# Kernel optimization log

Hardware: AMD Instinct MI355X
Metric: run time of the kernel (lower is better)

The kernel has to match this reference:

```python
import jax, jax.numpy as jnp
import numpy as np

N, B, F_DIM, K, DEG = 102400, 64, 64, 16, 8
E = N * DEG
PER_G = N // B  # equal-size graphs -> to_dense_batch is a reshape
EPS = 1e-15


def setup_inputs() -> dict:
    key = jax.random.key(0)
    k1, k2, k3, k4 = jax.random.split(key, 4)
    node_attr = jax.random.normal(k1, (N, F_DIM), dtype=jnp.float32)
    W = jax.random.normal(k2, (F_DIM, K), dtype=jnp.float32) * 0.1
    b = jnp.zeros((K,), dtype=jnp.float32)
    row = jax.random.randint(k3, (E,), 0, N)
    # receivers constrained to the sender's graph (block structure)
    col = (row // PER_G) * PER_G + jax.random.randint(k4, (E,), 0, PER_G)
    edge_index = jnp.stack([row, col]).astype(jnp.int32)
    batch = jnp.repeat(jnp.arange(B, dtype=jnp.int32), PER_G)
    return {"node_attr": node_attr, "W": W, "b": b,
            "edge_index": edge_index, "batch": batch, "num_graphs": B}


def reference(node_attr, W, b, edge_index, batch, num_graphs):
    n, f = node_attr.shape
    k = W.shape[1]
    per_g = n // num_graphs
    # selection = softmax(Linear(node_attr))            [N, K]
    sel = jax.nn.softmax(node_attr @ W + b, axis=-1)
    s = sel.reshape(num_graphs, per_g, k)               # to_dense_batch (equal graphs)
    row, col = edge_index[0], edge_index[1]
    # edge_pooling: outer product per edge, scatter-add by graph of sender
    assign_edge = sel[row][:, :, None] * sel[col][:, None, :]       # [E, K, K]
    dense_adj = jax.ops.segment_sum(assign_edge, batch[row], num_segments=num_graphs)  # [B, K, K]
    # normalize_adj (remove_self_loops=False)
    d = jnp.sqrt(dense_adj.sum(-1))[:, None, :] + EPS   # [B, 1, K]
    dense_adj = dense_adj / d / jnp.swapaxes(d, 1, 2)
    # mincut loss
    mincut_num = jnp.trace(dense_adj, axis1=1, axis2=2)             # [B]
    deg = jax.ops.segment_sum(jnp.ones((row.shape[0],), node_attr.dtype), row, num_segments=n)
    d_flat = deg.reshape(num_graphs, per_g)                          # [B, Nmax]
    # trace(S^T diag(d) S) = sum_n d_n * sum_k s_nk^2
    mincut_den = jnp.einsum('bn,bnk,bnk->b', d_flat, s, s)
    mincut_loss = jnp.mean(-(mincut_num / mincut_den))
    # orthogonality loss
    ss = jnp.einsum('bnk,bnl->bkl', s, s)                            # [B, K, K]
    ss_norm = jnp.linalg.norm(ss, axis=(-2, -1), keepdims=True)
    i_s = jnp.eye(k, dtype=ss.dtype)
    ortho = jnp.linalg.norm(ss / ss_norm - i_s / jnp.sqrt(jnp.asarray(k, ss.dtype)), axis=(-2, -1))
    ortho_loss = jnp.mean(ortho)
    # node_pooling: scatter of sel ⊗ node_attr by graph, flattened over (B, K)
    x = node_attr.reshape(num_graphs, per_g, f)
    cluster_node_attr = jnp.einsum('bnk,bnf->bkf', s, x).reshape(num_graphs * k, f)
    return cluster_node_attr, dense_adj, mincut_loss, ortho_loss
```

## Files before the change

### kernel.cpp

```cpp
#include <hip/hip_runtime.h>

#define F_DIMC 64
#define K_DIMC 16
#define NGRAPH 64
#define NXCD 8
#define SX_SPLIT 16
#define NB_SEL 400
#define NB_CHUNK 256
#define NB_ZERO 64
#define CHUNK_I4 800
#define ADJ_BLOCKS 256
#define ADJ_OFF (NGRAPH * K_DIMC * F_DIMC)
#define LOSS_OFF (ADJ_OFF + NGRAPH * K_DIMC * K_DIMC)
#define ZERO_BYTES 394240

typedef __attribute__((ext_vector_type(8))) short s16x8;
typedef __attribute__((ext_vector_type(4))) float f32x4;


__device__ inline unsigned short f2bf(float f) {
    unsigned u = __builtin_bit_cast(unsigned, f);
    u += 0x7fffu + ((u >> 16) & 1u);
    return (unsigned short)(u >> 16);
}

__global__ __launch_bounds__(256) void k_sel_hist(const float* __restrict__ node_attr,
                                                  const float* __restrict__ W,
                                                  const float* __restrict__ bias,
                                                  const int* __restrict__ row,
                                                  float* __restrict__ sel,
                                                  int* __restrict__ blockhist,
                                                  float4* __restrict__ zdst,
                                                  int N, int perG) {
    int t = threadIdx.x;
    if (blockIdx.x < NB_SEL) {
        __shared__ float sW[K_DIMC][F_DIMC];
        __shared__ float sb[K_DIMC];
        for (int idx = t; idx < F_DIMC * K_DIMC; idx += 256) {
            int f = idx / K_DIMC, k = idx % K_DIMC;
            sW[k][f] = W[idx];
        }
        if (t < K_DIMC) sb[t] = bias[t];
        __syncthreads();
        int n = blockIdx.x * 256 + t;
        if (n >= N) return;

        const float4* xr = (const float4*)(node_attr + (size_t)n * F_DIMC);
        float4 x[F_DIMC / 4];
#pragma unroll
        for (int f4 = 0; f4 < F_DIMC / 4; ++f4) x[f4] = xr[f4];

        float logits[K_DIMC];
#pragma unroll
        for (int k = 0; k < K_DIMC; ++k) {
            const float4* wk = (const float4*)&sW[k][0];
            float acc = sb[k];
#pragma unroll
            for (int f4 = 0; f4 < F_DIMC / 4; ++f4) {
                float4 w = wk[f4];
                acc += x[f4].x * w.x + x[f4].y * w.y + x[f4].z * w.z + x[f4].w * w.w;
            }
            logits[k] = acc;
        }
        float m = logits[0];
#pragma unroll
        for (int k = 1; k < K_DIMC; ++k) m = fmaxf(m, logits[k]);
        float sum = 0.f;
#pragma unroll
        for (int k = 0; k < K_DIMC; ++k) {
            float e = __expf(logits[k] - m);
            logits[k] = e;
            sum += e;
        }
        float inv = 1.f / sum;
        float4* sd = (float4*)(sel + (size_t)n * K_DIMC);
#pragma unroll
        for (int k4 = 0; k4 < K_DIMC / 4; ++k4) {
            float4 v;
            v.x = logits[4 * k4 + 0] * inv;
            v.y = logits[4 * k4 + 1] * inv;
            v.z = logits[4 * k4 + 2] * inv;
            v.w = logits[4 * k4 + 3] * inv;
            sd[k4] = v;
        }
    } else if (blockIdx.x < NB_SEL + NB_CHUNK) {
        __shared__ int lh[NGRAPH];
        int h = blockIdx.x - NB_SEL;
        if (t < NGRAPH) lh[t] = 0;
        __syncthreads();
        for (int i = t; i < CHUNK_I4; i += 256) {
            int4 r4 = ((const int4*)row)[h * CHUNK_I4 + i];
            atomicAdd(&lh[r4.x / perG], 1);
            atomicAdd(&lh[r4.y / perG], 1);
            atomicAdd(&lh[r4.z / perG], 1);
            atomicAdd(&lh[r4.w / perG], 1);
        }
        __syncthreads();
        if (t < NGRAPH) blockhist[h * NGRAPH + t] = lh[t];
    } else {
        int z = blockIdx.x - NB_SEL - NB_CHUNK;
        for (int i = z * 256 + t; i < ZERO_BYTES / 16; i += NB_ZERO * 256)
            zdst[i] = make_float4(0.f, 0.f, 0.f, 0.f);
    }
}

__global__ __launch_bounds__(256) void k_chunkscan(const int* __restrict__ blockhist,
                                                   int* __restrict__ chunkbase,
                                                   int* __restrict__ gtot) {
    int g = blockIdx.x;
    int t = threadIdx.x;
    int lane = t & 63;
    int wid = t >> 6;
    int v = blockhist[t * NGRAPH + g];
    int s = v;
#pragma unroll
    for (int d = 1; d < 64; d <<= 1) {
        int o = __shfl_up(s, d);
        if (lane >= d) s += o;
    }
    __shared__ int wsum[4];
    if (lane == 63) wsum[wid] = s;
    __syncthreads();
    int pre = 0;
#pragma unroll
    for (int w = 0; w < 4; ++w) pre += (w < wid) ? wsum[w] : 0;
    int incl = s + pre;
    chunkbase[t * NGRAPH + g] = incl - v;
    if (t == 255) gtot[g] = incl;
}

__global__ __launch_bounds__(256) void k_scatter_sx(const int* __restrict__ row,
                                                    const int* __restrict__ col,
                                                    const int* __restrict__ gtot,
                                                    const int* __restrict__ chunkbase,
                                                    int* __restrict__ offsets,
                                                    uint2* __restrict__ sorted,
                                                    const float* __restrict__ sel,
                                                    const float* __restrict__ x,
                                                    float* __restrict__ ssbuf,
                                                    float* __restrict__ sxbuf,
                                                    int perG) {
    int b = blockIdx.x;
    int r5 = b % 5;
    int t = threadIdx.x;
    if (r5 == 0) {
        __shared__ int base_[NGRAPH];
        __shared__ int lcnt[NGRAPH];
        int h = b / 5;
        if (t < 64) {
            int v = gtot[t];
            int s = v;
#pragma unroll
            for (int d = 1; d < 64; d <<= 1) {
                int o = __shfl_up(s, d);
                if (t >= d) s += o;
            }
            int offs = s - v;
            base_[t] = offs + chunkbase[h * NGRAPH + t];
            lcnt[t] = 0;
            if (h == 0) offsets[t] = offs;
        }
        __syncthreads();
        for (int i = t; i < CHUNK_I4; i += 256) {
            int e4 = h * CHUNK_I4 + i;
            int4 r4 = ((const int4*)row)[e4];
            int4 c4 = ((const int4*)col)[e4];
            int rr[4] = {r4.x, r4.y, r4.z, r4.w};
            int cc[4] = {c4.x, c4.y, c4.z, c4.w};
#pragma unroll
            for (int u = 0; u < 4; ++u) {
                int g = rr[u] / perG;
                int lpos = atomicAdd(&lcnt[g], 1);
                sorted[(size_t)base_[g] + lpos] = make_uint2((unsigned)rr[u], (unsigned)cc[u]);
            }
        }
    } else {
        int s = (b / 5) * 4 + (r5 - 1);
        int xcd = s & (NXCD - 1);
        int rem = s >> 3;
        int g = xcd * (NGRAPH / NXCD) + (rem >> 4);
        int split = rem & (SX_SPLIT - 1);
        int wid = t >> 6;
        int wslot = split * 4 + wid;
        int lane = t & 63;
        int k = lane >> 2;
        int sub = lane & 3;
        int f0 = sub * 16;
        int j0 = sub * 4;
        float accss[4] = {0.f, 0.f, 0.f, 0.f};
        float accsx[16];
#pragma unroll
        for (int j = 0; j < 16; ++j) accsx[j] = 0.f;
        size_t base = (size_t)g * perG;
#pragma unroll 2
        for (int nn = wslot; nn < perG; nn += 64) {
            size_t node = base + nn;
            float a = sel[node * K_DIMC + k];
            float4 s4 = *(const float4*)(sel + node * K_DIMC + j0);
            accss[0] += a * s4.x;
            accss[1] += a * s4.y;
            accss[2] += a * s4.z;
            accss[3] += a * s4.w;
            const float4* xv = (const float4*)(x + node * F_DIMC + f0);
#pragma unroll
            for (int j = 0; j < 4; ++j) {
                float4 v = xv[j];
                accsx[4 * j + 0] += a * v.x;
                accsx[4 * j + 1] += a * v.y;
                accsx[4 * j + 2] += a * v.z;
                accsx[4 * j + 3] += a * v.w;
            }
        }
        __shared__ float lsx[4][K_DIMC * F_DIMC];
        __shared__ float lss[4][256];
#pragma unroll
        for (int j4 = 0; j4 < 4; ++j4) {
            *(float4*)&lsx[wid][k * F_DIMC + f0 + 4 * j4] =
                make_float4(accsx[4 * j4], accsx[4 * j4 + 1], accsx[4 * j4 + 2], accsx[4 * j4 + 3]);
        }
        *(float4*)&lss[wid][k * K_DIMC + j0] = make_float4(accss[0], accss[1], accss[2], accss[3]);
        __syncthreads();
        for (int c = t; c < K_DIMC * F_DIMC; c += 256) {
            float sm = lsx[0][c] + lsx[1][c] + lsx[2][c] + lsx[3][c];
            atomicAdd(sxbuf + (size_t)g * (K_DIMC * F_DIMC) + c, sm);
        }
        {
            float sm = lss[0][t] + lss[1][t] + lss[2][t] + lss[3][t];
            atomicAdd(ssbuf + g * 256 + t, sm);
        }
    }
}

__global__ __launch_bounds__(256) void k_adj(const uint2* __restrict__ sorted,
                                             const int* __restrict__ offsets,
                                             const int* __restrict__ gtot,
                                             const float* __restrict__ sel,
                                             float* __restrict__ dense_raw,
                                             float* __restrict__ den) {
    __shared__ unsigned short At[4][512];
    __shared__ unsigned short Bt[4][512];
    __shared__ float lacc[4][256];
    __shared__ float qred[4];
    int b = blockIdx.x;
    int xcd = b & (NXCD - 1);
    int idx = b >> 3;
    int g = xcd * (NGRAPH / NXCD) + (idx >> 2);
    int split = idx & 3;
    int t = threadIdx.x;
    int wid = t >> 6;
    int lane = t & 63;
    int m = lane & 15;
    int grp = lane >> 4;
    int half8 = (lane & 1) * 8;

    int start = offsets[g];
    int cnt = gtot[g];
    int wslot = split * 4 + wid;
    f32x4 acc = {0.f, 0.f, 0.f, 0.f};
    float qacc = 0.f;
    int nch = (cnt + 31) >> 5;
    for (int ch = wslot; ch < nch; ch += 16) {
        int e0 = ch << 5;
        int eIdx = e0 + (lane >> 1);
        s16x8 av8 = {0, 0, 0, 0, 0, 0, 0, 0};
        s16x8 bv8 = {0, 0, 0, 0, 0, 0, 0, 0};
        if (eIdx < cnt) {
            uint2 pr = sorted[start + eIdx];
            const float4* ra = (const float4*)(sel + (size_t)pr.x * K_DIMC + half8);
            float4 a0 = ra[0], a1 = ra[1];
            qacc += a0.x * a0.x + a0.y * a0.y + a0.z * a0.z + a0.w * a0.w
                  + a1.x * a1.x + a1.y * a1.y + a1.z * a1.z + a1.w * a1.w;
            av8[0] = (short)f2bf(a0.x); av8[1] = (short)f2bf(a0.y);
            av8[2] = (short)f2bf(a0.z); av8[3] = (short)f2bf(a0.w);
            av8[4] = (short)f2bf(a1.x); av8[5] = (short)f2bf(a1.y);
            av8[6] = (short)f2bf(a1.z); av8[7] = (short)f2bf(a1.w);
            const float4* rb = (const float4*)(sel + (size_t)pr.y * K_DIMC + half8);
            float4 b0 = rb[0], b1 = rb[1];
            bv8[0] = (short)f2bf(b0.x); bv8[1] = (short)f2bf(b0.y);
            bv8[2] = (short)f2bf(b0.z); bv8[3] = (short)f2bf(b0.w);
            bv8[4] = (short)f2bf(b1.x); bv8[5] = (short)f2bf(b1.y);
            bv8[6] = (short)f2bf(b1.z); bv8[7] = (short)f2bf(b1.w);
        }
        ((s16x8*)At[wid])[lane] = av8;
        ((s16x8*)Bt[wid])[lane] = bv8;
        s16x8 av, bv;
#pragma unroll
        for (int d = 0; d < 8; ++d) {
            int off = (8 * grp + d) * K_DIMC + m;
            av[d] = (short)At[wid][off];
            bv[d] = (short)Bt[wid][off];
        }
        acc = __builtin_amdgcn_mfma_f32_16x16x32_bf16(av, bv, acc, 0, 0, 0);
    }
#pragma unroll
    for (int d = 0; d < 4; ++d) {
        lacc[wid][(4 * grp + d) * K_DIMC + m] = acc[d];
    }
#pragma unroll
    for (int off = 32; off > 0; off >>= 1) qacc += __shfl_down(qacc, off);
    if (lane == 0) qred[wid] = qacc;
    __syncthreads();
    float s = lacc[0][t] + lacc[1][t] + lacc[2][t] + lacc[3][t];
    atomicAdd(dense_raw + g * 256 + t, s);
    if (t == 0) {
        atomicAdd(den + g, qred[0] + qred[1] + qred[2] + qred[3]);
    }
}

__global__ __launch_bounds__(256) void k_fin(const float* __restrict__ dense_raw,
                                             const float* __restrict__ ssbuf,
                                             const float* __restrict__ sxbuf,
                                             const float* __restrict__ den,
                                             float* __restrict__ lossws,
                                             int* __restrict__ donecnt,
                                             float* __restrict__ out) {
    int g = blockIdx.x;
    int c = threadIdx.x;
    int k = c >> 4, j = c & 15;
    int lane = threadIdx.x & 63;
    int wid = threadIdx.x >> 6;

    ((float4*)(out + (size_t)g * (K_DIMC * F_DIMC)))[c] =
        ((const float4*)(sxbuf + (size_t)g * (K_DIMC * F_DIMC)))[c];

    float a = dense_raw[g * 256 + c];
    float s = a;
    s += __shfl_xor(s, 1);
    s += __shfl_xor(s, 2);
    s += __shfl_xor(s, 4);
    s += __shfl_xor(s, 8);
    __shared__ float dvrow[K_DIMC];
    if (j == 0) dvrow[k] = sqrtf(s) + 1e-15f;
    __syncthreads();
    float v = a / (dvrow[k] * dvrow[j]);
    out[ADJ_OFF + g * 256 + c] = v;

    float ss = ssbuf[g * 256 + c];
    float tt = (k == j) ? v : 0.f;
    float n2 = ss * ss;
#pragma unroll
    for (int off = 32; off > 0; off >>= 1) {
        tt += __shfl_down(tt, off);
        n2 += __shfl_down(n2, off);
    }
    __shared__ float redt[4], redn[4];
    if (lane == 0) { redt[wid] = tt; redn[wid] = n2; }
    __syncthreads();
    float tr = redt[0] + redt[1] + redt[2] + redt[3];
    float nrm2 = redn[0] + redn[1] + redn[2] + redn[3];
    float invn = 1.f / sqrtf(nrm2);
    float d = ss * invn - ((k == j) ? 0.25f : 0.f);
    float o2 = d * d;
#pragma unroll
    for (int off = 32; off > 0; off >>= 1) o2 += __shfl_down(o2, off);
    __shared__ float redo[4];
    if (lane == 0) redo[wid] = o2;
    __syncthreads();
    if (threadIdx.x == 0) {
        float osum = redo[0] + redo[1] + redo[2] + redo[3];
        float og = sqrtf(osum);
        float mterm = -(tr / den[g]);
        atomicAdd(lossws + 0, mterm * (1.f / NGRAPH));
        atomicAdd(lossws + 1, og * (1.f / NGRAPH));
        __threadfence();
        int old = atomicAdd(donecnt, 1);
        if (old == NGRAPH - 1) {
            float l0 = atomicAdd(lossws + 0, 0.f);
            float l1 = atomicAdd(lossws + 1, 0.f);
            out[LOSS_OFF + 0] = l0;
            out[LOSS_OFF + 1] = l1;
        }
    }
}

extern "C" void kernel_launch(void* const* d_in, const int* in_sizes, int n_in,
                              void* d_out, int out_size, void* d_ws, size_t ws_size,
                              hipStream_t stream) {
    const float* node_attr = (const float*)d_in[0];
    const float* W = (const float*)d_in[1];
    const float* bias = (const float*)d_in[2];
    const int* edge_index = (const int*)d_in[3];
    int N = in_sizes[0] / F_DIMC;
    int E = in_sizes[3] / 2;
    int perG = N / NGRAPH;
    const int* row = edge_index;
    const int* col = edge_index + E;
    float* out = (float*)d_out;
    char* ws = (char*)d_ws;

    float* den = (float*)(ws + 0);
    int* donecnt = (int*)(ws + 256);
    float* lossws = (float*)(ws + 512);
    float* dense_raw = (float*)(ws + 1024);
    float* ssbuf = (float*)(ws + 66560);
    float* sxbuf = (float*)(ws + 132096);
    int* offsets = (int*)(ws + 394240);
    int* gtot = (int*)(ws + 394496);
    int* blockhist = (int*)(ws + 394752);
    int* chunkbase = (int*)(ws + 460288);
    float* sel = (float*)(ws + 525824);
    uint2* sorted = (uint2*)(ws + 7079424);

    k_sel_hist<<<NB_SEL + NB_CHUNK + NB_ZERO, 256, 0, stream>>>(node_attr, W, bias, row, sel,
                                                                blockhist, (float4*)ws, N, perG);
    k_chunkscan<<<NGRAPH, 256, 0, stream>>>(blockhist, chunkbase, gtot);
    k_scatter_sx<<<NB_CHUNK * 5, 256, 0, stream>>>(row, col, gtot, chunkbase, offsets,
                                                   sorted, sel, node_attr, ssbuf, sxbuf, perG);
    k_adj<<<ADJ_BLOCKS, 256, 0, stream>>>(sorted, offsets, gtot, sel, dense_raw, den);
    k_fin<<<NGRAPH, 256, 0, stream>>>(dense_raw, ssbuf, sxbuf, den, lossws, donecnt, out);
}
```

Measured before the change: 86.33 us.

## Fuse finalize kernel into adjacency kernel via last-block counter, double adjacency splits

Removes the separate k_fin launch. Each k_adj block bumps a per-graph completion counter after its atomic accumulation, and the last of the 8 blocks for a graph does the normalization, the sx copy and the loss reduction. Adjacency work is also split over 512 blocks instead of 256, with 8 splits per graph, to expose more parallelism. This trades a kernel launch and its tail for extra atomics and a cross-block ordering dependence on the gdone counters, which rely on the workspace being zeroed each call.

```diff
diff --git a/kernel.cpp b/kernel.cpp
--- a/kernel.cpp
+++ b/kernel.cpp
@@ -9,7 +9,7 @@
 #define NB_CHUNK 256
 #define NB_ZERO 64
 #define CHUNK_I4 800
-#define ADJ_BLOCKS 256
+#define ADJ_BLOCKS 512
 #define ADJ_OFF (NGRAPH * K_DIMC * F_DIMC)
 #define LOSS_OFF (ADJ_OFF + NGRAPH * K_DIMC * K_DIMC)
 #define ZERO_BYTES 394240
@@ -236,16 +236,23 @@
                                              const int* __restrict__ gtot,
                                              const float* __restrict__ sel,
                                              float* __restrict__ dense_raw,
-                                             float* __restrict__ den) {
+                                             float* __restrict__ den,
+                                             const float* __restrict__ ssbuf,
+                                             const float* __restrict__ sxbuf,
+                                             float* __restrict__ lossws,
+                                             int* __restrict__ donecnt,
+                                             int* __restrict__ gdone,
+                                             float* __restrict__ out) {
     __shared__ unsigned short At[4][512];
     __shared__ unsigned short Bt[4][512];
     __shared__ float lacc[4][256];
     __shared__ float qred[4];
+    __shared__ int lastFlag;
     int b = blockIdx.x;
     int xcd = b & (NXCD - 1);
     int idx = b >> 3;
-    int g = xcd * (NGRAPH / NXCD) + (idx >> 2);
-    int split = idx & 3;
+    int g = xcd * (NGRAPH / NXCD) + (idx >> 3);
+    int split = idx & 7;
     int t = threadIdx.x;
     int wid = t >> 6;
     int lane = t & 63;
@@ -259,7 +266,7 @@
     f32x4 acc = {0.f, 0.f, 0.f, 0.f};
     float qacc = 0.f;
     int nch = (cnt + 31) >> 5;
-    for (int ch = wslot; ch < nch; ch += 16) {
+    for (int ch = wslot; ch < nch; ch += 32) {
         int e0 = ch << 5;
         int eIdx = e0 + (lane >> 1);
         s16x8 av8 = {0, 0, 0, 0, 0, 0, 0, 0};
@@ -304,71 +311,67 @@
     atomicAdd(dense_raw + g * 256 + t, s);
     if (t == 0) {
         atomicAdd(den + g, qred[0] + qred[1] + qred[2] + qred[3]);
-    }
-}
-
-__global__ __launch_bounds__(256) void k_fin(const float* __restrict__ dense_raw,
-                                             const float* __restrict__ ssbuf,
-                                             const float* __restrict__ sxbuf,
-                                             const float* __restrict__ den,
-                                             float* __restrict__ lossws,
-                                             int* __restrict__ donecnt,
-                                             float* __restrict__ out) {
-    int g = blockIdx.x;
-    int c = threadIdx.x;
-    int k = c >> 4, j = c & 15;
-    int lane = threadIdx.x & 63;
-    int wid = threadIdx.x >> 6;
-
-    ((float4*)(out + (size_t)g * (K_DIMC * F_DIMC)))[c] =
-        ((const float4*)(sxbuf + (size_t)g * (K_DIMC * F_DIMC)))[c];
-
-    float a = dense_raw[g * 256 + c];
-    float s = a;
-    s += __shfl_xor(s, 1);
-    s += __shfl_xor(s, 2);
-    s += __shfl_xor(s, 4);
-    s += __shfl_xor(s, 8);
-    __shared__ float dvrow[K_DIMC];
-    if (j == 0) dvrow[k] = sqrtf(s) + 1e-15f;
+        __threadfence();
+        int old = atomicAdd(&gdone[g], 1);
+        lastFlag = (old == 7);
+    }
     __syncthreads();
-    float v = a / (dvrow[k] * dvrow[j]);
-    out[ADJ_OFF + g * 256 + c] = v;
-
-    float ss = ssbuf[g * 256 + c];
-    float tt = (k == j) ? v : 0.f;
-    float n2 = ss * ss;
-#pragma unroll
-    for (int off = 32; off > 0; off >>= 1) {
-        tt += __shfl_down(tt, off);
-        n2 += __shfl_down(n2, off);
-    }
-    __shared__ float redt[4], redn[4];
-    if (lane == 0) { redt[wid] = tt; redn[wid] = n2; }
-    __syncthreads();
-    float tr = redt[0] + redt[1] + redt[2] + redt[3];
-    float nrm2 = redn[0] + redn[1] + redn[2] + redn[3];
-    float invn = 1.f / sqrtf(nrm2);
-    float d = ss * invn - ((k == j) ? 0.25f : 0.f);
-    float o2 = d * d;
-#pragma unroll
-    for (int off = 32; off > 0; off >>= 1) o2 += __shfl_down(o2, off);
-    __shared__ float redo[4];
-    if (lane == 0) redo[wid] = o2;
-    __syncthreads();
-    if (threadIdx.x == 0) {
-        float osum = redo[0] + redo[1] + redo[2] + redo[3];
-        float og = sqrtf(osum);
-        float mterm = -(tr / den[g]);
-        atomicAdd(lossws + 0, mterm * (1.f / NGRAPH));
-        atomicAdd(lossws + 1, og * (1.f / NGRAPH));
-        __threadfence();
-        int old = atomicAdd(donecnt, 1);
-        if (old == NGRAPH - 1) {
-            float l0 = atomicAdd(lossws + 0, 0.f);
-            float l1 = atomicAdd(lossws + 1, 0.f);
-            out[LOSS_OFF + 0] = l0;
-            out[LOSS_OFF + 1] = l1;
+    if (!lastFlag) return;
+
+    {
+        int c = t;
+        int k = c >> 4, j = c & 15;
+
+        ((float4*)(out + (size_t)g * (K_DIMC * F_DIMC)))[c] =
+            ((const float4*)(sxbuf + (size_t)g * (K_DIMC * F_DIMC)))[c];
+
+        float a = dense_raw[g * 256 + c];
+        float rs = a;
+        rs += __shfl_xor(rs, 1);
+        rs += __shfl_xor(rs, 2);
+        rs += __shfl_xor(rs, 4);
+        rs += __shfl_xor(rs, 8);
+        __shared__ float dvrow[K_DIMC];
+        if (j == 0) dvrow[k] = sqrtf(rs) + 1e-15f;
+        __syncthreads();
+        float v = a / (dvrow[k] * dvrow[j]);
+        out[ADJ_OFF + g * 256 + c] = v;
+
+        float ss = ssbuf[g * 256 + c];
+        float tt = (k == j) ? v : 0.f;
+        float n2 = ss * ss;
+#pragma unroll
+        for (int off = 32; off > 0; off >>= 1) {
+            tt += __shfl_down(tt, off);
+            n2 += __shfl_down(n2, off);
+        }
+        __shared__ float redt[4], redn[4];
+        if (lane == 0) { redt[wid] = tt; redn[wid] = n2; }
+        __syncthreads();
+        float tr = redt[0] + redt[1] + redt[2] + redt[3];
+        float nrm2 = redn[0] + redn[1] + redn[2] + redn[3];
+        float invn = 1.f / sqrtf(nrm2);
+        float dd = ss * invn - ((k == j) ? 0.25f : 0.f);
+        float o2 = dd * dd;
+#pragma unroll
+        for (int off = 32; off > 0; off >>= 1) o2 += __shfl_down(o2, off);
+        __shared__ float redo[4];
+        if (lane == 0) redo[wid] = o2;
+        __syncthreads();
+        if (t == 0) {
+            float osum = redo[0] + redo[1] + redo[2] + redo[3];
+            float og = sqrtf(osum);
+            float mterm = -(tr / den[g]);
+            atomicAdd(lossws + 0, mterm * (1.f / NGRAPH));
+            atomicAdd(lossws + 1, og * (1.f / NGRAPH));
+            __threadfence();
+            int old = atomicAdd(donecnt, 1);
+            if (old == NGRAPH - 1) {
+                float l0 = atomicAdd(lossws + 0, 0.f);
+                float l1 = atomicAdd(lossws + 1, 0.f);
+                out[LOSS_OFF + 0] = l0;
+                out[LOSS_OFF + 1] = l1;
+            }
         }
     }
 }
@@ -391,6 +394,7 @@
     float* den = (float*)(ws + 0);
     int* donecnt = (int*)(ws + 256);
     float* lossws = (float*)(ws + 512);
+    int* gdone = (int*)(ws + 768);
     float* dense_raw = (float*)(ws + 1024);
     float* ssbuf = (float*)(ws + 66560);
     float* sxbuf = (float*)(ws + 132096);
@@ -406,6 +410,6 @@
     k_chunkscan<<<NGRAPH, 256, 0, stream>>>(blockhist, chunkbase, gtot);
     k_scatter_sx<<<NB_CHUNK * 5, 256, 0, stream>>>(row, col, gtot, chunkbase, offsets,
                                                    sorted, sel, node_attr, ssbuf, sxbuf, perG);
-    k_adj<<<ADJ_BLOCKS, 256, 0, stream>>>(sorted, offsets, gtot, sel, dense_raw, den);
-    k_fin<<<NGRAPH, 256, 0, stream>>>(dense_raw, ssbuf, sxbuf, den, lossws, donecnt, out);
-}
+    k_adj<<<ADJ_BLOCKS, 256, 0, stream>>>(sorted, offsets, gtot, sel, dense_raw, den,
+                                          ssbuf, sxbuf, lossws, donecnt, gdone, out);
+}
```

New measurement: 83.94 us (median of 2 runs). -2.8%, faster.
